# Optimization experiments

Measured on AMD Instinct MI355X. Metric: run time of the kernel, lower is better.

## Reference

```python
import jax, jax.numpy as jnp
import numpy as np

DM = 512; NH = 8; EL = 3; FACTOR = 3; EPS = 1e-5

def layernorm(x, g, b):
    m = x.mean(-1, keepdims=True)
    v = x.var(-1, keepdims=True)
    return (x - m) / jnp.sqrt(v + EPS) * g + b

def pos_embed(L, d):
    pos = jnp.arange(L, dtype=jnp.float32)[:, None]
    div = jnp.exp(jnp.arange(0, d, 2, dtype=jnp.float32) * (-np.log(10000.0) / d))
    pe = jnp.zeros((L, d), jnp.float32)
    pe = pe.at[:, 0::2].set(jnp.sin(pos * div))
    pe = pe.at[:, 1::2].set(jnp.cos(pos * div))
    return pe

def circ_conv1d(x, w, b=None):
    # x: [B,L,Cin], w: [Cout,Cin,3]; torch Conv1d padding=1, padding_mode='circular'
    xp = jnp.concatenate([x[:, -1:], x, x[:, :1]], axis=1)
    y = jax.lax.conv_general_dilated(xp, w, (1,), 'VALID', dimension_numbers=('NWC', 'OIW', 'NWC'))
    return y if b is None else y + b

def prob_attention(q, k, v, rng):
    # q,k,v: [B,H,L,D] -- Informer ProbSparse attention (non-masked encoder case)
    B, H, L, D = q.shape
    LK = k.shape[2]
    U = min(int(FACTOR * np.ceil(np.log(LK))), LK)   # sampled keys per query
    u = min(int(FACTOR * np.ceil(np.log(L))), L)     # top queries kept
    idx = jax.random.randint(rng, (L, U), 0, LK)     # shared across B,H as in torch
    k_samp = k[:, :, idx]                            # [B,H,L,U,D]
    qk = jnp.einsum('bhld,bhlud->bhlu', q, k_samp)
    M = qk.max(-1) - qk.sum(-1) / LK                 # sparsity measure
    top = jax.lax.top_k(M, u)[1]                     # [B,H,u]
    q_red = jnp.take_along_axis(q, top[..., None], axis=2)
    scores = jnp.einsum('bhud,bhkd->bhuk', q_red, k) / jnp.sqrt(jnp.asarray(D, q.dtype))
    attn = jax.nn.softmax(scores, axis=-1)
    upd = jnp.einsum('bhuk,bhkd->bhud', attn, v)
    ctx = jnp.broadcast_to(v.mean(axis=2, keepdims=True), (B, H, L, D))
    bi = jnp.arange(B)[:, None, None]
    hi = jnp.arange(H)[None, :, None]
    return ctx.at[bi, hi, top].set(upd)

def encoder_layer(x, p, rng):
    Wq_, bq_, Wk_, bk_, Wv_, bv_, Wo_, bo_, w1, b1, w2, b2, g1, be1, g2, be2 = p
    B, L, _ = x.shape
    D = DM // NH
    q = (x @ Wq_.T + bq_).reshape(B, L, NH, D).transpose(0, 2, 1, 3)
    k = (x @ Wk_.T + bk_).reshape(B, L, NH, D).transpose(0, 2, 1, 3)
    v = (x @ Wv_.T + bv_).reshape(B, L, NH, D).transpose(0, 2, 1, 3)
    ctx = prob_attention(q, k, v, rng).transpose(0, 2, 1, 3).reshape(B, L, DM)
    x = x + (ctx @ Wo_.T + bo_)
    x = layernorm(x, g1, be1)
    y = jax.nn.gelu(x @ w1.T + b1, approximate=False)  # pointwise conv1 (k=1)
    y = y @ w2.T + b2                                   # pointwise conv2 (k=1)
    return layernorm(x + y, g2, be2)

def distil_layer(x, w, b, g, beta):
    y = circ_conv1d(x, w, b)                 # Conv1d k=3 circular
    mu = y.mean((0, 1))
    var = y.var((0, 1))                      # BatchNorm1d, training stats
    y = (y - mu) / jnp.sqrt(var + EPS) * g + beta
    y = jax.nn.elu(y)
    # MaxPool1d(kernel=3, stride=2, padding=1)
    return jax.lax.reduce_window(y, -jnp.inf, jax.lax.max, (1, 3, 1), (1, 2, 1), ((0, 0), (1, 1), (0, 0)))

def setup_inputs():
    key = jax.random.key(0)
    ks = jax.random.split(key, 12)
    B, S, CIN, COUT, DFF = 8, 2048, 7, 7, 2048
    r = lambda k, s: jax.random.normal(k, s, jnp.float32)
    return {
        'x_enc': r(ks[0], (B, S, CIN)),
        'tok_w': r(ks[1], (DM, CIN, 3)) * (2.0 / (CIN * 3)) ** 0.5,
        'Wq': r(ks[2], (EL, DM, DM)) * DM ** -0.5, 'bq': jnp.zeros((EL, DM)),
        'Wk': r(ks[3], (EL, DM, DM)) * DM ** -0.5, 'bk': jnp.zeros((EL, DM)),
        'Wv': r(ks[4], (EL, DM, DM)) * DM ** -0.5, 'bv': jnp.zeros((EL, DM)),
        'Wo': r(ks[5], (EL, DM, DM)) * DM ** -0.5, 'bo': jnp.zeros((EL, DM)),
        'conv1_w': r(ks[6], (EL, DFF, DM)) * DM ** -0.5, 'conv1_b': jnp.zeros((EL, DFF)),
        'conv2_w': r(ks[7], (EL, DM, DFF)) * DFF ** -0.5, 'conv2_b': jnp.zeros((EL, DM)),
        'ln1_g': jnp.ones((EL, DM)), 'ln1_b': jnp.zeros((EL, DM)),
        'ln2_g': jnp.ones((EL, DM)), 'ln2_b': jnp.zeros((EL, DM)),
        'dconv_w': r(ks[8], (EL - 1, DM, DM, 3)) * (DM * 3) ** -0.5, 'dconv_b': jnp.zeros((EL - 1, DM)),
        'bn_g': jnp.ones((EL - 1, DM)), 'bn_b': jnp.zeros((EL - 1, DM)),
        'lnf_g': jnp.ones((DM,)), 'lnf_b': jnp.zeros((DM,)),
        'end_w': r(ks[9], (COUT, DM)) * DM ** -0.5, 'end_b': jnp.zeros((COUT,)),
    }

def reference(x_enc, tok_w, Wq, bq, Wk, bk, Wv, bv, Wo, bo, conv1_w, conv1_b, conv2_w, conv2_b, ln1_g, ln1_b, ln2_g, ln2_b, dconv_w, dconv_b, bn_g, bn_b, lnf_g, lnf_b, end_w, end_b):
    x = circ_conv1d(x_enc, tok_w) + pos_embed(x_enc.shape[1], DM)  # DataEmbedding
    base = jax.random.key(42)
    for l in range(EL):
        p = (Wq[l], bq[l], Wk[l], bk[l], Wv[l], bv[l], Wo[l], bo[l],
             conv1_w[l], conv1_b[l], conv2_w[l], conv2_b[l],
             ln1_g[l], ln1_b[l], ln2_g[l], ln2_b[l])
        x = encoder_layer(x, p, jax.random.fold_in(base, l))
        if l < EL - 1:
            x = distil_layer(x, dconv_w[l], dconv_b[l], bn_g[l], bn_b[l])
    x = layernorm(x, lnf_g, lnf_b)
    return x @ end_w.T + end_b  # end_conv2 (Conv1d k=1)
```

## Files before the change

kernel.cpp:

```cpp
#include <hip/hip_runtime.h>
#include <cstdint>
#include <cstddef>

#define DMODEL 512
#define NHEAD 8
#define HD 64

typedef float f32x4 __attribute__((ext_vector_type(4)));
typedef _Float16 f16x8 __attribute__((ext_vector_type(8)));
typedef _Float16 f16x4 __attribute__((ext_vector_type(4)));

__device__ __forceinline__ uint32_t rotl32(uint32_t x, int r) {
  return (x << r) | (x >> (32 - r));
}

__device__ __forceinline__ void tf_block(uint32_t k0, uint32_t k1,
                                         uint32_t& x0, uint32_t& x1) {
  uint32_t ks0 = k0, ks1 = k1, ks2 = k0 ^ k1 ^ 0x1BD11BDAu;
  x0 += ks0; x1 += ks1;
  x0 += x1; x1 = rotl32(x1, 13); x1 ^= x0;
  x0 += x1; x1 = rotl32(x1, 15); x1 ^= x0;
  x0 += x1; x1 = rotl32(x1, 26); x1 ^= x0;
  x0 += x1; x1 = rotl32(x1, 6);  x1 ^= x0;
  x0 += ks1; x1 += ks2 + 1u;
  x0 += x1; x1 = rotl32(x1, 17); x1 ^= x0;
  x0 += x1; x1 = rotl32(x1, 29); x1 ^= x0;
  x0 += x1; x1 = rotl32(x1, 16); x1 ^= x0;
  x0 += x1; x1 = rotl32(x1, 24); x1 ^= x0;
  x0 += ks2; x1 += ks0 + 2u;
  x0 += x1; x1 = rotl32(x1, 13); x1 ^= x0;
  x0 += x1; x1 = rotl32(x1, 15); x1 ^= x0;
  x0 += x1; x1 = rotl32(x1, 26); x1 ^= x0;
  x0 += x1; x1 = rotl32(x1, 6);  x1 ^= x0;
  x0 += ks0; x1 += ks1 + 3u;
  x0 += x1; x1 = rotl32(x1, 17); x1 ^= x0;
  x0 += x1; x1 = rotl32(x1, 29); x1 ^= x0;
  x0 += x1; x1 = rotl32(x1, 16); x1 ^= x0;
  x0 += x1; x1 = rotl32(x1, 24); x1 ^= x0;
  x0 += ks1; x1 += ks2 + 4u;
  x0 += x1; x1 = rotl32(x1, 13); x1 ^= x0;
  x0 += x1; x1 = rotl32(x1, 15); x1 ^= x0;
  x0 += x1; x1 = rotl32(x1, 26); x1 ^= x0;
  x0 += x1; x1 = rotl32(x1, 6);  x1 ^= x0;
  x0 += ks2; x1 += ks0 + 5u;
}

__global__ void idx_kernel(int* __restrict__ idxb, int n, int layer, int mask) {
  int e = blockIdx.x * 256 + threadIdx.x;
  if (e >= n) return;
  uint32_t f0 = 0u, f1 = (uint32_t)layer;
  tf_block(0u, 42u, f0, f1);
  uint32_t s0 = 0u, s1 = 1u;
  tf_block(f0, f1, s0, s1);
  uint32_t x0 = 0u, x1 = (uint32_t)e;
  tf_block(s0, s1, x0, x1);
  uint32_t bits = x0 ^ x1;
  idxb[e] = (int)(bits & (uint32_t)mask);
}

__device__ __forceinline__ float gelu_f(float v) {
  return 0.5f * v * (1.0f + erff(v * 0.7071067811865476f));
}

template <int ACT, int HASR, int CONV, int PART>
__global__ __launch_bounds__(256, 4) void gemm128(
    const float* __restrict__ A, const void* __restrict__ Wsp,
    const float* __restrict__ bias, const float* Rres, float* C,
    int N, int K, int Lmask, int ntx, int nty, int kloop, int ks) {
  __shared__ __align__(16) _Float16 smA[2][64][32];
  __shared__ __align__(16) _Float16 smW[2][128][32];
  const _Float16* Wh = (const _Float16*)Wsp;
  const _Float16* Wl = Wh + (size_t)N * K;
  const int tid = threadIdx.x;
  int blk = blockIdx.x;
  const int tiles = ntx * nty;
  int kb = 0;
  if (PART) { kb = blk / tiles; blk -= kb * tiles; }
  const int koff = kb * kloop;
  const int xcd = blk & 7;
  const int j = blk >> 3;
  const int jr = j / ntx;
  const int row_t = xcd * (nty >> 3) + jr;
  const int col_t = j - jr * ntx;
  const int row0 = row_t * 64, col0 = col_t * 128;

  const int r4 = tid >> 2;
  const int ss = tid & 3;

  const float* Ap = A + (size_t)(row0 + r4) * K + koff + ss * 8;
  const _Float16* Wh0 = Wh + (size_t)(col0 + r4) * K + koff + ss * 8;
  const _Float16* Wh1 = Wh + (size_t)(col0 + 64 + r4) * K + koff + ss * 8;
  const _Float16* Wl0 = Wl + (size_t)(col0 + r4) * K + koff + ss * 8;
  const _Float16* Wl1 = Wl + (size_t)(col0 + 64 + r4) * K + koff + ss * 8;
  int tcv = 0, bb = 0;
  if (CONV) {
    int a0 = row0 + r4;
    tcv = a0 & Lmask; bb = a0 & ~Lmask;
  }

  const int lane = tid & 63;
  const int wv = tid >> 6;
  const int wc = wv << 5;
  const int fr = lane & 15;
  const int fs = lane >> 4;

  f32x4 acc[4][2];
  {
    f32x4 z = {0.f, 0.f, 0.f, 0.f};
#pragma unroll
    for (int r = 0; r < 4; ++r)
#pragma unroll
      for (int c = 0; c < 2; ++c) acc[r][c] = z;
  }

  f32x4 ra[2], rwh[2], rwl[2];
  f16x8 wfh[2], wfl[2], afh[4], afl[4];

  auto gload = [&](int k0) {
    const float* ap;
    if (CONV) {
      int kabs = koff + k0 + ss * 8;
      int w = kabs >> 9, cq = kabs & 511;
      ap = A + (size_t)(bb | ((tcv - 1 + w) & Lmask)) * 512 + cq;
    } else {
      ap = Ap + k0;
    }
    ra[0] = *(const f32x4*)(ap);
    ra[1] = *(const f32x4*)(ap + 4);
    rwh[0] = *(const f32x4*)(Wh0 + k0);
    rwh[1] = *(const f32x4*)(Wh1 + k0);
    rwl[0] = *(const f32x4*)(Wl0 + k0);
    rwl[1] = *(const f32x4*)(Wl1 + k0);
  };

  auto stage = [&]() {
    {
      const int sl = (ss ^ ((r4 >> 1) & 3)) << 3;
      float tmp[8];
      *(f32x4*)(tmp) = ra[0];
      *(f32x4*)(tmp + 4) = ra[1];
      _Float16 hv[8], lv[8];
#pragma unroll
      for (int q = 0; q < 8; ++q) {
        _Float16 h = (_Float16)tmp[q];
        hv[q] = h;
        lv[q] = (_Float16)(tmp[q] - (float)h);
      }
      *(f16x8*)&smA[0][r4][sl] = *(f16x8*)hv;
      *(f16x8*)&smA[1][r4][sl] = *(f16x8*)lv;
    }
#pragma unroll
    for (int p = 0; p < 2; ++p) {
      const int row = (p << 6) + r4;
      const int sl = (ss ^ ((row >> 1) & 3)) << 3;
      *(f32x4*)&smW[0][row][sl] = rwh[p];
      *(f32x4*)&smW[1][row][sl] = rwl[p];
    }
  };

  auto readfrags = [&]() {
#pragma unroll
    for (int c = 0; c < 2; ++c) {
      const int row = wc + (c << 4) + fr;
      const int sl = (fs ^ ((row >> 1) & 3)) << 3;
      wfh[c] = *(const f16x8*)&smW[0][row][sl];
      wfl[c] = *(const f16x8*)&smW[1][row][sl];
    }
#pragma unroll
    for (int r = 0; r < 4; ++r) {
      const int row = (r << 4) + fr;
      const int sl = (fs ^ ((row >> 1) & 3)) << 3;
      afh[r] = *(const f16x8*)&smA[0][row][sl];
      afl[r] = *(const f16x8*)&smA[1][row][sl];
    }
  };

  const int T = kloop >> 5;
  gload(0);

  for (int it = 0; it < T; ++it) {
    stage();
    __syncthreads();
    if (it + 1 < T) gload((it + 1) << 5);
    readfrags();
    __builtin_amdgcn_s_setprio(1);
#pragma unroll
    for (int r = 0; r < 4; ++r)
#pragma unroll
      for (int c = 0; c < 2; ++c)
        acc[r][c] = __builtin_amdgcn_mfma_f32_16x16x32_f16(afh[r], wfh[c],
                                                           acc[r][c], 0, 0, 0);
#pragma unroll
    for (int r = 0; r < 4; ++r)
#pragma unroll
      for (int c = 0; c < 2; ++c)
        acc[r][c] = __builtin_amdgcn_mfma_f32_16x16x32_f16(afh[r], wfl[c],
                                                           acc[r][c], 0, 0, 0);
#pragma unroll
    for (int r = 0; r < 4; ++r)
#pragma unroll
      for (int c = 0; c < 2; ++c)
        acc[r][c] = __builtin_amdgcn_mfma_f32_16x16x32_f16(afl[r], wfh[c],
                                                           acc[r][c], 0, 0, 0);
    __builtin_amdgcn_s_setprio(0);
    __syncthreads();
  }

  const int crow = fs << 2;
  if (PART) {
    float* Cp = C + (size_t)kb * ((size_t)(nty << 6)) * N;
#pragma unroll
    for (int r = 0; r < 4; ++r) {
      const int m0 = row0 + (r << 4) + crow;
#pragma unroll
      for (int c = 0; c < 2; ++c) {
        const int n0 = col0 + wc + (c << 4) + fr;
#pragma unroll
        for (int q = 0; q < 4; ++q)
          Cp[(size_t)(m0 + q) * N + n0] = acc[r][c][q];
      }
    }
  } else {
#pragma unroll
    for (int r = 0; r < 4; ++r) {
      const int m0 = row0 + (r << 4) + crow;
#pragma unroll
      for (int c = 0; c < 2; ++c) {
        const int n0 = col0 + wc + (c << 4) + fr;
        const float bcol = bias[n0];
#pragma unroll
        for (int q = 0; q < 4; ++q) {
          float v = acc[r][c][q] + bcol;
          if (HASR) v += Rres[(size_t)(m0 + q) * N + n0];
          if (ACT == 1) v = gelu_f(v);
          C[(size_t)(m0 + q) * N + n0] = v;
        }
      }
    }
  }
}

template <int HASR>
__global__ __launch_bounds__(256) void combine_kernel(
    const float* __restrict__ part, const float* __restrict__ bias,
    const float* Rres, float* __restrict__ Cout, size_t MN, int ks) {
  size_t gid = (size_t)blockIdx.x * 256 + threadIdx.x;
  int c = (int)(gid & 511);
  float v = 0.f;
  for (int kb = 0; kb < ks; kb++) v += part[kb * MN + gid];
  v += bias[c];
  if (HASR) v += Rres[gid];
  Cout[gid] = v;
}

__global__ __launch_bounds__(256) void splitw_kernel(const float* __restrict__ w,
                                                     _Float16* __restrict__ o,
                                                     int n) {
  int g = (blockIdx.x * 256 + threadIdx.x) << 2;
  if (g >= n) return;
  f32x4 f = *(const f32x4*)(w + g);
  f16x4 hv, lv;
#pragma unroll
  for (int q = 0; q < 4; ++q) {
    _Float16 h = (_Float16)f[q];
    hv[q] = h;
    lv[q] = (_Float16)(f[q] - (float)h);
  }
  *(f16x4*)(o + g) = hv;
  *(f16x4*)(o + n + g) = lv;
}

__global__ void tokpe_kernel(const float* __restrict__ xe,
                             const float* __restrict__ w,
                             float* __restrict__ out, int S) {
  int gid = blockIdx.x * 256 + threadIdx.x;
  int o = gid & 511;
  int bt = gid >> 9;
  int t = bt % S, b = bt / S;
  float acc = 0.f;
#pragma unroll
  for (int ww = 0; ww < 3; ww++) {
    int tt = t - 1 + ww;
    tt = (tt < 0) ? tt + S : (tt >= S ? tt - S : tt);
    const float* xr = xe + ((size_t)(b * S + tt)) * 7;
#pragma unroll
    for (int i = 0; i < 7; i++) acc += xr[i] * w[o * 21 + i * 3 + ww];
  }
  int i2 = o >> 1;
  float dv = expf((float)(2 * i2) * (-9.210340371976184f / 512.0f));
  float ang = (float)t * dv;
  acc += (o & 1) ? cosf(ang) : sinf(ang);
  out[gid] = acc;
}

__global__ void packw_kernel(const float* __restrict__ dw,
                             _Float16* __restrict__ wp) {
  int gid = blockIdx.x * 256 + threadIdx.x;
  int o = gid / 1536;
  int kk = gid - o * 1536;
  int ww = kk / 512;
  int c = kk - ww * 512;
  float v = dw[((size_t)o * 512 + c) * 3 + ww];
  _Float16 h = (_Float16)v;
  wp[gid] = h;
  wp[786432 + gid] = (_Float16)(v - (float)h);
}

__global__ __launch_bounds__(256, 8) void mscore_kernel(
    const float* __restrict__ Q, const float* __restrict__ Kb,
    const int* __restrict__ idxb, float* __restrict__ Mout, int L, int U) {
  int i = blockIdx.x;
  int b = i & 7;
  int j = i >> 3;
  int tid = threadIdx.x;
  int qd = tid >> 2;
  int q = tid & 3;
  int h = qd & 7;
  int t = j * 8 + (qd >> 3);
  const float* qp = Q + ((size_t)(b * L + t)) * DMODEL + h * HD + q * 4;
  float4 qv0 = *(const float4*)(qp);
  float4 qv1 = *(const float4*)(qp + 16);
  float4 qv2 = *(const float4*)(qp + 32);
  float4 qv3 = *(const float4*)(qp + 48);
  const float* Kh = Kb + (size_t)b * L * DMODEL + h * HD + q * 4;
  const int* ip = idxb + t * U;
  float mx = -3.4e38f, sm = 0.f;
  int kr = ip[0];
  for (int jj = 0; jj < U; jj++) {
    const float* kp = Kh + (size_t)kr * DMODEL;
    float4 k0 = *(const float4*)(kp);
    float4 k1 = *(const float4*)(kp + 16);
    float4 k2 = *(const float4*)(kp + 32);
    float4 k3 = *(const float4*)(kp + 48);
    if (jj + 1 < U) kr = ip[jj + 1];
    float d = qv0.x * k0.x + qv0.y * k0.y + qv0.z * k0.z + qv0.w * k0.w +
              qv1.x * k1.x + qv1.y * k1.y + qv1.z * k1.z + qv1.w * k1.w +
              qv2.x * k2.x + qv2.y * k2.y + qv2.z * k2.z + qv2.w * k2.w +
              qv3.x * k3.x + qv3.y * k3.y + qv3.z * k3.z + qv3.w * k3.w;
    d += __shfl_xor(d, 1);
    d += __shfl_xor(d, 2);
    mx = fmaxf(mx, d);
    sm += d;
  }
  if (q == 0) Mout[(size_t)(b * 8 + h) * L + t] = mx - sm / (float)L;
}

__global__ __launch_bounds__(256) void topk_kernel(const float* __restrict__ Mv,
                                                   int* __restrict__ topb, int L,
                                                   int u) {
  __shared__ float wv_s[4];
  __shared__ int wi_s[4];
  __shared__ int best_s;
  int bh = blockIdx.x, tid = threadIdx.x;
  int lane = tid & 63, w = tid >> 6;
  int cnt = L >> 8;
  float lv[8];
  for (int i = 0; i < cnt; i++) lv[i] = Mv[(size_t)bh * L + i * 256 + tid];
  for (int r = 0; r < u; r++) {
    float bv = -3.4e38f;
    int bi = 0x7fffffff;
    for (int i = 0; i < cnt; i++) {
      if (lv[i] > bv) { bv = lv[i]; bi = i * 256 + tid; }
    }
    for (int s = 32; s > 0; s >>= 1) {
      float ov = __shfl_down(bv, s);
      int oi = __shfl_down(bi, s);
      if (ov > bv || (ov == bv && oi < bi)) { bv = ov; bi = oi; }
    }
    if (lane == 0) { wv_s[w] = bv; wi_s[w] = bi; }
    __syncthreads();
    if (tid == 0) {
      float fv = wv_s[0];
      int fi = wi_s[0];
      for (int q = 1; q < 4; q++) {
        if (wv_s[q] > fv || (wv_s[q] == fv && wi_s[q] < fi)) {
          fv = wv_s[q];
          fi = wi_s[q];
        }
      }
      best_s = fi;
      topb[bh * u + r] = fi;
    }
    __syncthreads();
    int win = best_s;
    if ((win & 255) == tid) lv[win >> 8] = -3.4e38f;
  }
}

__global__ void gatherq_kernel(const float* __restrict__ Q,
                               const int* __restrict__ topb,
                               float* __restrict__ qsel, int L, int u) {
  int i = blockIdx.x;
  int bh = i / u;
  int b = bh >> 3, h = bh & 7;
  int t = topb[i];
  qsel[i * HD + threadIdx.x] =
      Q[((size_t)(b * L + t)) * DMODEL + h * HD + threadIdx.x];
}

__global__ __launch_bounds__(256) void xmean_kernel(const float* __restrict__ x,
                                                    float* __restrict__ psumx,
                                                    int L) {
  int i = blockIdx.x;
  int b = i >> 3, g = i & 7;
  int rows = L >> 3;
  int tid = threadIdx.x;
  const float* base = x + ((size_t)b * L + (size_t)g * rows) * DMODEL;
  float s0 = 0.f, s1 = 0.f;
  for (int t = 0; t < rows; t++) {
    s0 += base[(size_t)t * DMODEL + tid];
    s1 += base[(size_t)t * DMODEL + tid + 256];
  }
  psumx[i * DMODEL + tid] = s0;
  psumx[i * DMODEL + tid + 256] = s1;
}

__global__ __launch_bounds__(256) void mvmake_kernel(
    const float* __restrict__ psumx, const float* __restrict__ Wv,
    const float* __restrict__ bv, const float* __restrict__ Wo,
    const float* __restrict__ bo, float* __restrict__ mvg,
    float* __restrict__ mvWog, int L) {
  __shared__ float xm[512];
  __shared__ float mvs[512];
  int b = blockIdx.x, tid = threadIdx.x;
  float inv = 1.0f / (float)L;
  for (int nn = 0; nn < 2; nn++) {
    int c = tid + nn * 256;
    float s = 0.f;
    for (int g = 0; g < 8; g++) s += psumx[(b * 8 + g) * DMODEL + c];
    xm[c] = s * inv;
  }
  __syncthreads();
  for (int nn = 0; nn < 2; nn++) {
    int n = tid + nn * 256;
    const float* wr = Wv + (size_t)n * 512;
    float s = bv[n];
    for (int k = 0; k < 512; k += 4) {
      float4 w4 = *(const float4*)(wr + k);
      s += xm[k] * w4.x + xm[k + 1] * w4.y + xm[k + 2] * w4.z + xm[k + 3] * w4.w;
    }
    mvs[n] = s;
    mvg[b * DMODEL + n] = s;
  }
  __syncthreads();
  for (int nn = 0; nn < 2; nn++) {
    int n = tid + nn * 256;
    const float* wr = Wo + (size_t)n * 512;
    float s = bo[n];
    for (int k = 0; k < 512; k += 4) {
      float4 w4 = *(const float4*)(wr + k);
      s += mvs[k] * w4.x + mvs[k + 1] * w4.y + mvs[k + 2] * w4.z +
           mvs[k + 3] * w4.w;
    }
    mvWog[b * DMODEL + n] = s;
  }
}

__global__ void x1bcast_kernel(const float* __restrict__ x,
                               const float* __restrict__ mvWog,
                               float* __restrict__ x1, int L) {
  int gid = blockIdx.x * 256 + threadIdx.x;
  int c = gid & 511;
  int r = gid >> 9;
  int b = r / L;
  x1[gid] = x[gid] + mvWog[b * DMODEL + c];
}

__global__ __launch_bounds__(256) void attnflash_kernel(
    const float* __restrict__ qsel, const float* __restrict__ Kb,
    const float* __restrict__ Vb, float* __restrict__ pm,
    float* __restrict__ pl, float* __restrict__ pO, int L, int u, int nchunk) {
  __shared__ float qs[24][64];
  __shared__ float Kt[64][68];
  __shared__ float Ps[24][68];
  int blk = blockIdx.x;
  int bh = blk / nchunk;
  int c = blk - bh * nchunk;
  int b = bh >> 3, h = bh & 7;
  int cs = L / nchunk;
  int tid = threadIdx.x;
  int lane = tid & 63;
  int w = tid >> 6;
  for (int i = tid; i < u * 64; i += 256)
    qs[i >> 6][i & 63] = qsel[(size_t)bh * u * 64 + i];
  float m[6], l[6], O[6];
#pragma unroll
  for (int k = 0; k < 6; k++) { m[k] = -3.4e38f; l[k] = 0.f; O[k] = 0.f; }
  const float* Kbase = Kb + (size_t)b * L * DMODEL + h * HD;
  const float* Vbase = Vb + (size_t)b * L * DMODEL + h * HD;
  const int jrow = tid & 63;
  const int dch = (tid >> 6) << 4;
  for (int j0 = c * cs; j0 < (c + 1) * cs; j0 += 64) {
    __syncthreads();
    const float* kr = Kbase + (size_t)(j0 + jrow) * DMODEL + dch;
    float4 k0 = *(const float4*)(kr);
    float4 k1 = *(const float4*)(kr + 4);
    float4 k2 = *(const float4*)(kr + 8);
    float4 k3 = *(const float4*)(kr + 12);
#pragma unroll
    for (int q = 0; q < 4; q++) {
      Kt[dch + q][jrow] = ((float*)&k0)[q];
      Kt[dch + 4 + q][jrow] = ((float*)&k1)[q];
      Kt[dch + 8 + q][jrow] = ((float*)&k2)[q];
      Kt[dch + 12 + q][jrow] = ((float*)&k3)[q];
    }
    __syncthreads();
#pragma unroll
    for (int k = 0; k < 6; k++) {
      int qi = 4 * k + w;
      if (qi >= u) break;
      float s = 0.f;
#pragma unroll
      for (int d = 0; d < 64; d++) s += qs[qi][d] * Kt[d][lane];
      s *= 0.125f;
      float mx = s;
#pragma unroll
      for (int off = 32; off > 0; off >>= 1)
        mx = fmaxf(mx, __shfl_down(mx, off));
      mx = __shfl(mx, 0);
      float mnew = fmaxf(m[k], mx);
      float p = expf(s - mnew);
      float ps = p;
#pragma unroll
      for (int off = 32; off > 0; off >>= 1) ps += __shfl_down(ps, off);
      ps = __shfl(ps, 0);
      float alpha = expf(m[k] - mnew);
      l[k] = l[k] * alpha + ps;
      m[k] = mnew;
      O[k] *= alpha;
      Ps[qi][lane] = p;
    }
    for (int j = 0; j < 64; j += 4) {
      float v0 = Vbase[(size_t)(j0 + j) * DMODEL + lane];
      float v1 = Vbase[(size_t)(j0 + j + 1) * DMODEL + lane];
      float v2 = Vbase[(size_t)(j0 + j + 2) * DMODEL + lane];
      float v3 = Vbase[(size_t)(j0 + j + 3) * DMODEL + lane];
#pragma unroll
      for (int k = 0; k < 6; k++) {
        int qi = 4 * k + w;
        if (qi >= u) break;
        O[k] += Ps[qi][j] * v0 + Ps[qi][j + 1] * v1 + Ps[qi][j + 2] * v2 +
                Ps[qi][j + 3] * v3;
      }
    }
  }
#pragma unroll
  for (int k = 0; k < 6; k++) {
    int qi = 4 * k + w;
    if (qi < u) {
      int p = (bh * nchunk + c) * u + qi;
      if (lane == 0) { pm[p] = m[k]; pl[p] = l[k]; }
      pO[(size_t)p * 64 + lane] = O[k];
    }
  }
}

__global__ __launch_bounds__(256) void deltaWo_kernel(
    const float* __restrict__ pm, const float* __restrict__ pl,
    const float* __restrict__ pO, const float* __restrict__ mvg,
    const int* __restrict__ topb, const float* __restrict__ Wo, float* x1,
    int L, int u, int nchunk) {
  __shared__ float ds[64];
  int sel = blockIdx.x;
  int bh = sel / u;
  int qi = sel - bh * u;
  int b = bh >> 3, h = bh & 7;
  int t = topb[sel];
  int tid = threadIdx.x;
  if (tid < 64) {
    float mstar = -3.4e38f;
    for (int c = 0; c < nchunk; c++)
      mstar = fmaxf(mstar, pm[(bh * nchunk + c) * u + qi]);
    float lstar = 0.f, O = 0.f;
    for (int c = 0; c < nchunk; c++) {
      int p = (bh * nchunk + c) * u + qi;
      float wgt = expf(pm[p] - mstar);
      lstar += wgt * pl[p];
      O += wgt * pO[(size_t)p * 64 + tid];
    }
    ds[tid] = O / lstar - mvg[b * DMODEL + h * HD + tid];
  }
  __syncthreads();
  float* row = x1 + ((size_t)(b * L + t)) * DMODEL;
  for (int nn = 0; nn < 2; nn++) {
    int n = tid + nn * 256;
    const float* wr = Wo + (size_t)n * 512 + h * HD;
    float a = 0.f;
#pragma unroll
    for (int k = 0; k < 64; k += 4) {
      float4 w4 = *(const float4*)(wr + k);
      a += ds[k] * w4.x + ds[k + 1] * w4.y + ds[k + 2] * w4.z + ds[k + 3] * w4.w;
    }
    atomicAdd(row + n, a);
  }
}

__global__ __launch_bounds__(256) void ln_kernel(const float* __restrict__ X,
                                                 const float* __restrict__ g,
                                                 const float* __restrict__ bta,
                                                 float* __restrict__ Y) {
  int row = blockIdx.x * 4 + (threadIdx.x >> 6);
  int lane = threadIdx.x & 63;
  size_t base = (size_t)row * DMODEL + lane * 8;
  float4 a = *(const float4*)(X + base);
  float4 b = *(const float4*)(X + base + 4);
  float s = a.x + a.y + a.z + a.w + b.x + b.y + b.z + b.w;
#pragma unroll
  for (int off = 32; off > 0; off >>= 1) s += __shfl_xor(s, off);
  float mean = s * (1.0f / 512.0f);
  float d[8];
  d[0] = a.x - mean; d[1] = a.y - mean; d[2] = a.z - mean; d[3] = a.w - mean;
  d[4] = b.x - mean; d[5] = b.y - mean; d[6] = b.z - mean; d[7] = b.w - mean;
  float q = 0.f;
#pragma unroll
  for (int i = 0; i < 8; ++i) q += d[i] * d[i];
#pragma unroll
  for (int off = 32; off > 0; off >>= 1) q += __shfl_xor(q, off);
  float inv = 1.0f / sqrtf(q * (1.0f / 512.0f) + 1e-5f);
  int col = lane * 8;
  float4 g0 = *(const float4*)(g + col);
  float4 g1 = *(const float4*)(g + col + 4);
  float4 t0 = *(const float4*)(bta + col);
  float4 t1 = *(const float4*)(bta + col + 4);
  float4 y0, y1;
  y0.x = d[0] * inv * g0.x + t0.x; y0.y = d[1] * inv * g0.y + t0.y;
  y0.z = d[2] * inv * g0.z + t0.z; y0.w = d[3] * inv * g0.w + t0.w;
  y1.x = d[4] * inv * g1.x + t1.x; y1.y = d[5] * inv * g1.y + t1.y;
  y1.z = d[6] * inv * g1.z + t1.z; y1.w = d[7] * inv * g1.w + t1.w;
  *(float4*)(Y + base) = y0;
  *(float4*)(Y + base + 4) = y1;
}

__global__ __launch_bounds__(256) void bnpart_kernel(const float* __restrict__ z,
                                                     float* __restrict__ psum,
                                                     float* __restrict__ psq,
                                                     int rowsPer) {
  int blk = blockIdx.x, tid = threadIdx.x;
  size_t r0 = (size_t)blk * rowsPer;
  float s0 = 0, q0 = 0, s1 = 0, q1 = 0;
  for (int r = 0; r < rowsPer; r++) {
    const float* zp = z + (r0 + r) * DMODEL;
    float a = zp[tid];
    s0 += a; q0 += a * a;
    float c = zp[tid + 256];
    s1 += c; q1 += c * c;
  }
  psum[blk * DMODEL + tid] = s0;
  psum[blk * DMODEL + tid + 256] = s1;
  psq[blk * DMODEL + tid] = q0;
  psq[blk * DMODEL + tid + 256] = q1;
}

__global__ void bnfin_kernel(const float* __restrict__ psum,
                             const float* __restrict__ psq, float* __restrict__ mu,
                             float* __restrict__ var, int nb, int Rtot) {
  int c = blockIdx.x * 256 + threadIdx.x;
  float s = 0, q = 0;
  for (int b = 0; b < nb; b++) {
    s += psum[b * DMODEL + c];
    q += psq[b * DMODEL + c];
  }
  float m = s / (float)Rtot;
  mu[c] = m;
  var[c] = fmaxf(q / (float)Rtot - m * m, 0.f);
}

__global__ void bnpool_kernel(const float* __restrict__ z,
                              const float* __restrict__ mu,
                              const float* __restrict__ var,
                              const float* __restrict__ g,
                              const float* __restrict__ bta,
                              float* __restrict__ out, int L) {
  int gid = blockIdx.x * 256 + threadIdx.x;
  int c = gid & 511;
  int bt = gid >> 9;
  int L2 = L >> 1;
  int t2 = bt % L2, b = bt / L2;
  float m = mu[c];
  float inv = 1.0f / sqrtf(var[c] + 1e-5f);
  float gg = g[c], bb = bta[c];
  float best = -3.4e38f;
#pragma unroll
  for (int ww = 0; ww < 3; ww++) {
    int t = 2 * t2 - 1 + ww;
    if (t < 0 || t >= L) continue;
    float yv = (z[((size_t)(b * L + t)) * DMODEL + c] - m) * inv * gg + bb;
    yv = (yv > 0.f) ? yv : expm1f(yv);
    best = fmaxf(best, yv);
  }
  out[gid] = best;
}

__global__ __launch_bounds__(64) void end_kernel(const float* __restrict__ xn,
                                                 const float* __restrict__ ew,
                                                 const float* __restrict__ eb,
                                                 float* __restrict__ out) {
  __shared__ float xs[512];
  __shared__ float red[64];
  int row = blockIdx.x, tid = threadIdx.x;
#pragma unroll
  for (int i = 0; i < 8; i++) xs[tid + 64 * i] = xn[(size_t)row * DMODEL + tid + 64 * i];
  __syncthreads();
  for (int c = 0; c < 7; c++) {
    float p = 0.f;
    for (int d = tid; d < 512; d += 64) p += xs[d] * ew[c * DMODEL + d];
    red[tid] = p;
    __syncthreads();
    for (int s = 32; s > 0; s >>= 1) {
      if (tid < s) red[tid] += red[tid + s];
      __syncthreads();
    }
    if (tid == 0) out[row * 7 + c] = red[0] + eb[c];
    __syncthreads();
  }
}

extern "C" void kernel_launch(void* const* d_in, const int* in_sizes, int n_in,
                              void* d_out, int out_size, void* d_ws,
                              size_t ws_size, hipStream_t stream) {
  (void)in_sizes; (void)n_in; (void)out_size;
  const float* x_enc = (const float*)d_in[0];
  const float* tok_w = (const float*)d_in[1];
  const float* Wq = (const float*)d_in[2];
  const float* bq = (const float*)d_in[3];
  const float* Wk = (const float*)d_in[4];
  const float* bk = (const float*)d_in[5];
  const float* Wv = (const float*)d_in[6];
  const float* bv = (const float*)d_in[7];
  const float* Wo = (const float*)d_in[8];
  const float* bo = (const float*)d_in[9];
  const float* w1 = (const float*)d_in[10];
  const float* b1 = (const float*)d_in[11];
  const float* w2 = (const float*)d_in[12];
  const float* b2 = (const float*)d_in[13];
  const float* g1 = (const float*)d_in[14];
  const float* be1 = (const float*)d_in[15];
  const float* g2 = (const float*)d_in[16];
  const float* be2 = (const float*)d_in[17];
  const float* dw = (const float*)d_in[18];
  const float* db = (const float*)d_in[19];
  const float* bng = (const float*)d_in[20];
  const float* bnb = (const float*)d_in[21];
  const float* lnfg = (const float*)d_in[22];
  const float* lnfb = (const float*)d_in[23];
  const float* endw = (const float*)d_in[24];
  const float* endb = (const float*)d_in[25];
  float* out = (float*)d_out;
  char* ws = (char*)d_ws;

  const int NCHMAX = 32;

  size_t o = 0;
  float* buf0 = (float*)(ws + o); o += (size_t)16384 * 512 * 4;
  float* qbuf = (float*)(ws + o); o += (size_t)16384 * 512 * 4;
  float* kbuf = (float*)(ws + o); o += (size_t)16384 * 512 * 4;
  float* wpack = (float*)(ws + o); o += (size_t)512 * 1536 * 4;
  float* Mb    = (float*)(ws + o); o += (size_t)64 * 2048 * 4;
  int*   idxb  = (int*)(ws + o);   o += (size_t)2048 * 24 * 4;
  int*   topb  = (int*)(ws + o);   o += 8192;
  float* qsel  = (float*)(ws + o); o += (size_t)64 * 24 * 64 * 4;
  float* mvg   = (float*)(ws + o); o += (size_t)8 * 512 * 4;
  float* mvWog = (float*)(ws + o); o += (size_t)8 * 512 * 4;
  float* psumx = (float*)(ws + o); o += (size_t)64 * 512 * 4;
  float* psum  = (float*)(ws + o); o += (size_t)128 * 512 * 4;
  float* psq   = (float*)(ws + o); o += (size_t)128 * 512 * 4;
  float* muv   = (float*)(ws + o); o += 2048;
  float* varv  = (float*)(ws + o); o += 2048;
  float* pmb   = (float*)(ws + o); o += (size_t)64 * NCHMAX * 24 * 4;
  float* plb   = (float*)(ws + o); o += (size_t)64 * NCHMAX * 24 * 4;
  float* pOb   = (float*)(ws + o); o += (size_t)64 * NCHMAX * 24 * 64 * 4;
  _Float16* wqs = (_Float16*)(ws + o); o += (size_t)512 * 512 * 4;
  _Float16* w1s = (_Float16*)(ws + o); o += (size_t)2048 * 512 * 4;
  _Float16* w2s = (_Float16*)(ws + o); o += (size_t)512 * 2048 * 4;
  float* partb = (float*)(ws + o); o += (size_t)4 * 4096 * 2048;
  const bool uks = (ws_size >= o);

  const int B = 8;
  const int S = 2048;
  tokpe_kernel<<<B * S * DMODEL / 256, 256, 0, stream>>>(x_enc, tok_w, buf0, S);

  int L = S;
  const int Uarr[3] = {24, 21, 21};
  for (int l = 0; l < 3; l++) {
    int U = Uarr[l];
    int u = Uarr[l];
    int BL = B * L;
    int ntyQ = BL >> 6;
    size_t MN = (size_t)BL * 512;
    int gq = 4 * ntyQ;
    int ksq = (gq >= 1024 || !uks) ? 1 : (1024 / gq);
    int nch = L >> 6;
    idx_kernel<<<(L * U + 255) / 256, 256, 0, stream>>>(idxb, L * U, l, L - 1);

    splitw_kernel<<<256, 256, 0, stream>>>(Wq + (size_t)l * 262144, wqs, 262144);
    if (ksq == 1) {
      gemm128<0, 0, 0, 0><<<gq, 256, 0, stream>>>(
          buf0, wqs, bq + l * 512, nullptr, qbuf, 512, 512, 0, 4, ntyQ, 512, 1);
    } else {
      gemm128<0, 0, 0, 1><<<gq * ksq, 256, 0, stream>>>(
          buf0, wqs, nullptr, nullptr, partb, 512, 512, 0, 4, ntyQ, 512 / ksq,
          ksq);
      combine_kernel<0><<<(unsigned)(MN / 256), 256, 0, stream>>>(
          partb, bq + l * 512, nullptr, qbuf, MN, ksq);
    }
    splitw_kernel<<<256, 256, 0, stream>>>(Wk + (size_t)l * 262144, wqs, 262144);
    if (ksq == 1) {
      gemm128<0, 0, 0, 0><<<gq, 256, 0, stream>>>(
          buf0, wqs, bk + l * 512, nullptr, kbuf, 512, 512, 0, 4, ntyQ, 512, 1);
    } else {
      gemm128<0, 0, 0, 1><<<gq * ksq, 256, 0, stream>>>(
          buf0, wqs, nullptr, nullptr, partb, 512, 512, 0, 4, ntyQ, 512 / ksq,
          ksq);
      combine_kernel<0><<<(unsigned)(MN / 256), 256, 0, stream>>>(
          partb, bk + l * 512, nullptr, kbuf, MN, ksq);
    }
    mscore_kernel<<<L, 256, 0, stream>>>(qbuf, kbuf, idxb, Mb, L, U);
    topk_kernel<<<64, 256, 0, stream>>>(Mb, topb, L, u);
    gatherq_kernel<<<64 * u, 64, 0, stream>>>(qbuf, topb, qsel, L, u);
    xmean_kernel<<<64, 256, 0, stream>>>(buf0, psumx, L);
    mvmake_kernel<<<8, 256, 0, stream>>>(psumx, Wv + (size_t)l * 262144,
                                         bv + l * 512, Wo + (size_t)l * 262144,
                                         bo + l * 512, mvg, mvWog, L);
    splitw_kernel<<<256, 256, 0, stream>>>(Wv + (size_t)l * 262144, wqs, 262144);
    if (ksq == 1) {
      gemm128<0, 0, 0, 0><<<gq, 256, 0, stream>>>(
          buf0, wqs, bv + l * 512, nullptr, qbuf, 512, 512, 0, 4, ntyQ, 512, 1);
    } else {
      gemm128<0, 0, 0, 1><<<gq * ksq, 256, 0, stream>>>(
          buf0, wqs, nullptr, nullptr, partb, 512, 512, 0, 4, ntyQ, 512 / ksq,
          ksq);
      combine_kernel<0><<<(unsigned)(MN / 256), 256, 0, stream>>>(
          partb, bv + l * 512, nullptr, qbuf, MN, ksq);
    }
    attnflash_kernel<<<64 * nch, 256, 0, stream>>>(qsel, kbuf, qbuf, pmb, plb,
                                                   pOb, L, u, nch);
    x1bcast_kernel<<<(unsigned)(MN / 256), 256, 0, stream>>>(buf0, mvWog, kbuf, L);
    deltaWo_kernel<<<64 * u, 256, 0, stream>>>(pmb, plb, pOb, mvg, topb,
                                               Wo + (size_t)l * 262144, kbuf, L,
                                               u, nch);
    ln_kernel<<<BL / 4, 256, 0, stream>>>(kbuf, g1 + l * 512, be1 + l * 512, qbuf);
    splitw_kernel<<<1024, 256, 0, stream>>>(w1 + (size_t)l * 1048576, w1s,
                                            1048576);
    splitw_kernel<<<1024, 256, 0, stream>>>(w2 + (size_t)l * 1048576, w2s,
                                            1048576);
    for (int r0 = 0; r0 < BL; r0 += 4096) {
      gemm128<1, 0, 0, 0><<<16 * 64, 256, 0, stream>>>(
          qbuf + (size_t)r0 * 512, w1s, b1 + l * 2048, nullptr, buf0, 2048, 512,
          0, 16, 64, 512, 1);
      if (uks) {
        gemm128<0, 0, 0, 1><<<4 * 64 * 4, 256, 0, stream>>>(
            buf0, w2s, nullptr, nullptr, partb, 512, 2048, 0, 4, 64, 512, 4);
        combine_kernel<1><<<4096 * 512 / 256, 256, 0, stream>>>(
            partb, b2 + l * 512, qbuf + (size_t)r0 * 512,
            kbuf + (size_t)r0 * 512, (size_t)4096 * 512, 4);
      } else {
        gemm128<0, 1, 0, 0><<<4 * 64, 256, 0, stream>>>(
            buf0, w2s, b2 + l * 512, qbuf + (size_t)r0 * 512,
            kbuf + (size_t)r0 * 512, 512, 2048, 0, 4, 64, 2048, 1);
      }
    }
    ln_kernel<<<BL / 4, 256, 0, stream>>>(kbuf, g2 + l * 512, be2 + l * 512, buf0);

    if (l < 2) {
      packw_kernel<<<512 * 1536 / 256, 256, 0, stream>>>(
          dw + (size_t)l * 512 * 512 * 3, (_Float16*)wpack);
      int ksc = (gq >= 1024 || !uks) ? 1 : 2;
      if (ksc == 1) {
        gemm128<0, 0, 1, 0><<<gq, 256, 0, stream>>>(
            buf0, wpack, db + l * 512, nullptr, kbuf, 512, 1536, L - 1, 4, ntyQ,
            1536, 1);
      } else {
        gemm128<0, 0, 1, 1><<<gq * 2, 256, 0, stream>>>(
            buf0, wpack, nullptr, nullptr, partb, 512, 1536, L - 1, 4, ntyQ,
            768, 2);
        combine_kernel<0><<<(unsigned)(MN / 256), 256, 0, stream>>>(
            partb, db + l * 512, nullptr, kbuf, MN, 2);
      }
      int nb = BL / 128;
      bnpart_kernel<<<nb, 256, 0, stream>>>(kbuf, psum, psq, 128);
      bnfin_kernel<<<2, 256, 0, stream>>>(psum, psq, muv, varv, nb, BL);
      bnpool_kernel<<<(BL / 2) * 512 / 256, 256, 0, stream>>>(
          kbuf, muv, varv, bng + l * 512, bnb + l * 512, buf0, L);
      L >>= 1;
    }
  }
  int BL = B * L;
  ln_kernel<<<BL / 4, 256, 0, stream>>>(buf0, lnfg, lnfb, qbuf);
  end_kernel<<<BL, 64, 0, stream>>>(qbuf, endw, endb, out);
}
```

Before: 2.028 ms.

## Load weight fragments directly to registers and double-buffer the A tile in LDS

Each wave now reads its own W fragments (high and low fp16 halves) straight from global memory into registers instead of staging them through shared memory. The A tile becomes double-buffered in LDS, with a two-stage-ahead global prefetch, so there is one barrier per k-step instead of two. This cuts LDS traffic and synchronisation in the split-fp16 GEMM, but each wave now issues uncoalesced 16-byte global loads for W, with some redundancy across waves, and more registers are live.

```diff
diff --git a/kernel.cpp b/kernel.cpp
--- a/kernel.cpp
+++ b/kernel.cpp
@@ -67,8 +67,7 @@
     const float* __restrict__ A, const void* __restrict__ Wsp,
     const float* __restrict__ bias, const float* Rres, float* C,
     int N, int K, int Lmask, int ntx, int nty, int kloop, int ks) {
-  __shared__ __align__(16) _Float16 smA[2][64][32];
-  __shared__ __align__(16) _Float16 smW[2][128][32];
+  __shared__ __align__(16) _Float16 smA[2][2][64][32];
   const _Float16* Wh = (const _Float16*)Wsp;
   const _Float16* Wl = Wh + (size_t)N * K;
   const int tid = threadIdx.x;
@@ -86,12 +85,7 @@
 
   const int r4 = tid >> 2;
   const int ss = tid & 3;
-
   const float* Ap = A + (size_t)(row0 + r4) * K + koff + ss * 8;
-  const _Float16* Wh0 = Wh + (size_t)(col0 + r4) * K + koff + ss * 8;
-  const _Float16* Wh1 = Wh + (size_t)(col0 + 64 + r4) * K + koff + ss * 8;
-  const _Float16* Wl0 = Wl + (size_t)(col0 + r4) * K + koff + ss * 8;
-  const _Float16* Wl1 = Wl + (size_t)(col0 + 64 + r4) * K + koff + ss * 8;
   int tcv = 0, bb = 0;
   if (CONV) {
     int a0 = row0 + r4;
@@ -104,6 +98,11 @@
   const int fr = lane & 15;
   const int fs = lane >> 4;
 
+  const _Float16* wph0 = Wh + (size_t)(col0 + wc + fr) * K + koff + fs * 8;
+  const _Float16* wph1 = Wh + (size_t)(col0 + wc + 16 + fr) * K + koff + fs * 8;
+  const _Float16* wpl0 = Wl + (size_t)(col0 + wc + fr) * K + koff + fs * 8;
+  const _Float16* wpl1 = Wl + (size_t)(col0 + wc + 16 + fr) * K + koff + fs * 8;
+
   f32x4 acc[4][2];
   {
     f32x4 z = {0.f, 0.f, 0.f, 0.f};
@@ -113,10 +112,11 @@
       for (int c = 0; c < 2; ++c) acc[r][c] = z;
   }
 
-  f32x4 ra[2], rwh[2], rwl[2];
-  f16x8 wfh[2], wfl[2], afh[4], afl[4];
-
-  auto gload = [&](int k0) {
+  f32x4 ra[2];
+  f16x8 afh[4], afl[4];
+  f16x8 wch[2], wcl[2], wnh[2], wnl[2];
+
+  auto gloadA = [&](int k0) {
     const float* ap;
     if (CONV) {
       int kabs = koff + k0 + ss * 8;
@@ -127,83 +127,83 @@
     }
     ra[0] = *(const f32x4*)(ap);
     ra[1] = *(const f32x4*)(ap + 4);
-    rwh[0] = *(const f32x4*)(Wh0 + k0);
-    rwh[1] = *(const f32x4*)(Wh1 + k0);
-    rwl[0] = *(const f32x4*)(Wl0 + k0);
-    rwl[1] = *(const f32x4*)(Wl1 + k0);
   };
 
-  auto stage = [&]() {
-    {
-      const int sl = (ss ^ ((r4 >> 1) & 3)) << 3;
-      float tmp[8];
-      *(f32x4*)(tmp) = ra[0];
-      *(f32x4*)(tmp + 4) = ra[1];
-      _Float16 hv[8], lv[8];
-#pragma unroll
-      for (int q = 0; q < 8; ++q) {
-        _Float16 h = (_Float16)tmp[q];
-        hv[q] = h;
-        lv[q] = (_Float16)(tmp[q] - (float)h);
-      }
-      *(f16x8*)&smA[0][r4][sl] = *(f16x8*)hv;
-      *(f16x8*)&smA[1][r4][sl] = *(f16x8*)lv;
-    }
-#pragma unroll
-    for (int p = 0; p < 2; ++p) {
-      const int row = (p << 6) + r4;
-      const int sl = (ss ^ ((row >> 1) & 3)) << 3;
-      *(f32x4*)&smW[0][row][sl] = rwh[p];
-      *(f32x4*)&smW[1][row][sl] = rwl[p];
-    }
+  auto loadW = [&](int k0, f16x8* h, f16x8* l) {
+    h[0] = *(const f16x8*)(wph0 + k0);
+    h[1] = *(const f16x8*)(wph1 + k0);
+    l[0] = *(const f16x8*)(wpl0 + k0);
+    l[1] = *(const f16x8*)(wpl1 + k0);
   };
 
-  auto readfrags = [&]() {
-#pragma unroll
-    for (int c = 0; c < 2; ++c) {
-      const int row = wc + (c << 4) + fr;
-      const int sl = (fs ^ ((row >> 1) & 3)) << 3;
-      wfh[c] = *(const f16x8*)&smW[0][row][sl];
-      wfl[c] = *(const f16x8*)&smW[1][row][sl];
-    }
+  auto stageA = [&](int buf) {
+    const int sl = (ss ^ ((r4 >> 1) & 3)) << 3;
+    float tmp[8];
+    *(f32x4*)(tmp) = ra[0];
+    *(f32x4*)(tmp + 4) = ra[1];
+    _Float16 hv[8], lv[8];
+#pragma unroll
+    for (int q = 0; q < 8; ++q) {
+      _Float16 h = (_Float16)tmp[q];
+      hv[q] = h;
+      lv[q] = (_Float16)(tmp[q] - (float)h);
+    }
+    *(f16x8*)&smA[buf][0][r4][sl] = *(f16x8*)hv;
+    *(f16x8*)&smA[buf][1][r4][sl] = *(f16x8*)lv;
+  };
+
+  auto readA = [&](int buf) {
 #pragma unroll
     for (int r = 0; r < 4; ++r) {
       const int row = (r << 4) + fr;
       const int sl = (fs ^ ((row >> 1) & 3)) << 3;
-      afh[r] = *(const f16x8*)&smA[0][row][sl];
-      afl[r] = *(const f16x8*)&smA[1][row][sl];
+      afh[r] = *(const f16x8*)&smA[buf][0][row][sl];
+      afl[r] = *(const f16x8*)&smA[buf][1][row][sl];
     }
   };
 
   const int T = kloop >> 5;
-  gload(0);
+  gloadA(0);
+  stageA(0);
+  if (T > 1) gloadA(1 << 5);
+  loadW(0, wch, wcl);
+  __syncthreads();
+  readA(0);
+  int cur = 0;
 
   for (int it = 0; it < T; ++it) {
-    stage();
-    __syncthreads();
-    if (it + 1 < T) gload((it + 1) << 5);
-    readfrags();
+    if (it + 1 < T) {
+      stageA(cur ^ 1);
+      loadW((it + 1) << 5, wnh, wnl);
+    }
+    if (it + 2 < T) gloadA((it + 2) << 5);
     __builtin_amdgcn_s_setprio(1);
 #pragma unroll
     for (int r = 0; r < 4; ++r)
 #pragma unroll
       for (int c = 0; c < 2; ++c)
-        acc[r][c] = __builtin_amdgcn_mfma_f32_16x16x32_f16(afh[r], wfh[c],
+        acc[r][c] = __builtin_amdgcn_mfma_f32_16x16x32_f16(afh[r], wch[c],
                                                            acc[r][c], 0, 0, 0);
 #pragma unroll
     for (int r = 0; r < 4; ++r)
 #pragma unroll
       for (int c = 0; c < 2; ++c)
-        acc[r][c] = __builtin_amdgcn_mfma_f32_16x16x32_f16(afh[r], wfl[c],
+        acc[r][c] = __builtin_amdgcn_mfma_f32_16x16x32_f16(afh[r], wcl[c],
                                                            acc[r][c], 0, 0, 0);
 #pragma unroll
     for (int r = 0; r < 4; ++r)
 #pragma unroll
       for (int c = 0; c < 2; ++c)
-        acc[r][c] = __builtin_amdgcn_mfma_f32_16x16x32_f16(afl[r], wfh[c],
+        acc[r][c] = __builtin_amdgcn_mfma_f32_16x16x32_f16(afl[r], wch[c],
                                                            acc[r][c], 0, 0, 0);
     __builtin_amdgcn_s_setprio(0);
-    __syncthreads();
+    if (it + 1 < T) {
+      __syncthreads();
+      cur ^= 1;
+      readA(cur);
+      wch[0] = wnh[0]; wch[1] = wnh[1];
+      wcl[0] = wnl[0]; wcl[1] = wnl[1];
+    }
   }
 
   const int crow = fs << 2;
```

Result: slower. 2.230 ms (+10.0%).
